# Kernel tuning notes

Hardware: AMD Instinct MI355X
Metric: run time of the kernel (lower is better)

The kernel has to match this reference:

```python
import jax, jax.numpy as jnp
import numpy as np

N = 100000      # nodes
E = 800000      # edges (avg degree 8)
D_IN = 128
D_OUT = 128
HOPS = 3        # K in SGConv


def setup_inputs() -> dict:
    key = jax.random.key(0)
    k1, k2, k3 = jax.random.split(key, 3)
    x = jax.random.normal(k1, (N, D_IN), dtype=jnp.float32)
    edge_index = jax.random.randint(k2, (2, E), 0, N, dtype=jnp.int64)
    # SGConv's final torch.nn.Linear(in_channels, out_channels)
    W = jax.random.normal(k3, (D_OUT, D_IN), dtype=jnp.float32) / np.sqrt(D_IN).astype(np.float32)
    b = jnp.zeros((D_OUT,), dtype=jnp.float32)
    return {"x": x, "edge_index": edge_index, "W": W, "b": b}


def reference(x, edge_index, W, b):
    n = x.shape[0]
    loop = jnp.arange(n, dtype=edge_index.dtype)
    # gcn_norm with add_self_loops=True (SGConv default)
    src = jnp.concatenate([edge_index[0], loop])  # message sources
    dst = jnp.concatenate([edge_index[1], loop])  # aggregation targets
    ones = jnp.ones(src.shape[0], dtype=x.dtype)
    deg = jax.ops.segment_sum(ones, dst, num_segments=n)
    dinv = jnp.where(deg > 0, jax.lax.rsqrt(deg), 0.0)
    norm = dinv[src] * dinv[dst]  # symmetric D^-1/2 A_hat D^-1/2 coefficients

    def hop(h, _):
        msg = h[src] * norm[:, None]                      # [E+N, D] gather
        return jax.ops.segment_sum(msg, dst, num_segments=n), None

    h, _ = jax.lax.scan(hop, x, None, length=HOPS)        # A_norm^K x
    return h @ W.T + b                                     # final linear
```

## Files before the change

### kernel.cpp

```cpp
#include <hip/hip_runtime.h>
#include <hip/hip_bf16.h>

#define DF 128


typedef __attribute__((ext_vector_type(8))) short shortx8;
typedef __attribute__((ext_vector_type(4))) float floatx4;

__device__ __forceinline__ unsigned short f32_to_bf16_rne(float f) {
    unsigned int u = __float_as_uint(f);
    unsigned int r = (u >> 16) & 1u;
    u += 0x7FFFu + r;
    return (unsigned short)(u >> 16);
}
__device__ __forceinline__ float bf16_lo(unsigned int w) { return __uint_as_float(w << 16); }
__device__ __forceinline__ float bf16_hi(unsigned int w) { return __uint_as_float(w & 0xffff0000u); }
__device__ __forceinline__ unsigned int pack_bf16(float x, float y) {
    return ((unsigned int)f32_to_bf16_rne(y) << 16) | (unsigned int)f32_to_bf16_rne(x);
}

__global__ void detect_flags_kernel(const unsigned int* __restrict__ ew, int enwords,
                                    const unsigned short* __restrict__ xh, int xnh,
                                    int* __restrict__ flagI, int* __restrict__ flagD) {
    __shared__ int eodd_nz;
    __shared__ int xbig;
    if (threadIdx.x == 0) { eodd_nz = 0; xbig = 0; }
    __syncthreads();
    int f1 = 0;
    for (int i = 1 + 2 * (int)threadIdx.x; i < enwords; i += 2 * (int)blockDim.x)
        if (ew[i] != 0u) f1 = 1;
    int c = 0;
    for (int i = 2 * (int)threadIdx.x; i < xnh; i += 2 * (int)blockDim.x) {
        unsigned int e = ((unsigned int)xh[i] >> 7) & 0xFFu;
        if (e >= 0xC0u) c++;
    }
    if (f1) eodd_nz = 1;
    if (c) atomicAdd(&xbig, c);
    __syncthreads();
    if (threadIdx.x == 0) {
        *flagI = (eodd_nz == 0) ? 1 : 0;
        *flagD = (xbig > 8) ? 0 : 1;
    }
}

__global__ void count_deg_kernel(const int* __restrict__ eidx, const int* __restrict__ flagI,
                                 int E, int n, int* __restrict__ cnt) {
    int e = blockIdx.x * blockDim.x + threadIdx.x;
    if (e >= E) return;
    int s, d;
    if (*flagI) {
        const long long* p = (const long long*)eidx;
        s = (int)p[e];
        d = (int)p[(long long)E + e];
    } else {
        s = eidx[e];
        d = eidx[E + e];
    }
    if (d < 0 || d >= n || s < 0 || s >= n) return;
    atomicAdd(&cnt[d], 1);
}

__global__ void dinv_kernel(const int* __restrict__ cnt, float* __restrict__ dinv, int n) {
    int i = blockIdx.x * blockDim.x + threadIdx.x;
    if (i < n) dinv[i] = rsqrtf((float)(cnt[i] + 1));
}

__global__ void scan_blocks_kernel(const int* __restrict__ cnt, int* __restrict__ row_start,
                                   int* __restrict__ partials, int n) {
    __shared__ int s[256];
    int i = blockIdx.x * 256 + threadIdx.x;
    int v = (i < n) ? cnt[i] : 0;
    s[threadIdx.x] = v;
    __syncthreads();
    for (int off = 1; off < 256; off <<= 1) {
        int t = ((int)threadIdx.x >= off) ? s[threadIdx.x - off] : 0;
        __syncthreads();
        s[threadIdx.x] += t;
        __syncthreads();
    }
    if (i < n) row_start[i] = s[threadIdx.x] - v;
    if (threadIdx.x == 255) partials[blockIdx.x] = s[255];
}

__global__ void scan_partials_kernel(int* __restrict__ partials, int nparts) {
    __shared__ int s[512];
    int v = ((int)threadIdx.x < nparts) ? partials[threadIdx.x] : 0;
    s[threadIdx.x] = v;
    __syncthreads();
    for (int off = 1; off < 512; off <<= 1) {
        int t = ((int)threadIdx.x >= off) ? s[threadIdx.x - off] : 0;
        __syncthreads();
        s[threadIdx.x] += t;
        __syncthreads();
    }
    if ((int)threadIdx.x < nparts) partials[threadIdx.x] = s[threadIdx.x] - v;
}

__global__ void finalize_rows_kernel(int* __restrict__ row_start, const int* __restrict__ partials,
                                     const int* __restrict__ cnt, int* __restrict__ cursor, int n) {
    int i = blockIdx.x * 256 + threadIdx.x;
    if (i < n) {
        int r = row_start[i] + partials[blockIdx.x];
        row_start[i] = r;
        cursor[i] = r;
        if (i == n - 1) row_start[n] = r + cnt[i];
    }
}

__global__ void scatter_kernel(const int* __restrict__ eidx, const int* __restrict__ flagI,
                               int E, int n, const float* __restrict__ dinv,
                               int* __restrict__ cursor, int2* __restrict__ csr) {
    int e = blockIdx.x * blockDim.x + threadIdx.x;
    if (e >= E) return;
    int s, d;
    if (*flagI) {
        const long long* p = (const long long*)eidx;
        s = (int)p[e];
        d = (int)p[(long long)E + e];
    } else {
        s = eidx[e];
        d = eidx[E + e];
    }
    if (d < 0 || d >= n || s < 0 || s >= n) return;
    int pos = atomicAdd(&cursor[d], 1);
    int2 pk;
    pk.x = s;
    pk.y = __float_as_int(dinv[s]);
    csr[pos] = pk;
}

__global__ void cast_x_kernel(const void* __restrict__ x, uint2* __restrict__ xb,
                              const int* __restrict__ flagD, int nw2) {
    int i = blockIdx.x * blockDim.x + threadIdx.x;
    if (i >= nw2) return;
    if (*flagD) {
        xb[i] = ((const uint2*)x)[i];
    } else {
        float4 v = ((const float4*)x)[i];
        uint2 o;
        o.x = pack_bf16(v.x, v.y);
        o.y = pack_bf16(v.z, v.w);
        xb[i] = o;
    }
}

__global__ void cast_wb_kernel(const void* __restrict__ W, const void* __restrict__ b,
                               unsigned short* __restrict__ Wb, float* __restrict__ bias_f,
                               const int* __restrict__ flagD) {
    int i = blockIdx.x * 256 + threadIdx.x;
    int bf = *flagD;
    if (i < 128 * 128)
        Wb[i] = bf ? ((const unsigned short*)W)[i] : f32_to_bf16_rne(((const float*)W)[i]);
    if (i < 128)
        bias_f[i] = bf ? bf16_lo((unsigned int)((const unsigned short*)b)[i]) : ((const float*)b)[i];
}

__global__ __launch_bounds__(256) void hop_kernel(const uint4* __restrict__ hin,
                                                  uint4* __restrict__ hout,
                                                  const int2* __restrict__ csr,
                                                  const int* __restrict__ row_start,
                                                  const float* __restrict__ dinv, int n) {
    int gw = (int)((blockIdx.x * 256 + threadIdx.x) >> 6);
    int lane = (int)(threadIdx.x & 63);
    if (gw >= n) return;
    int e = lane >> 4, c = lane & 15;
    float di = dinv[gw];
    int beg = row_start[gw], end = row_start[gw + 1];
    uint4 sv = hin[(size_t)gw * 16 + c];
    float a0 = 0.f, a1 = 0.f, a2 = 0.f, a3 = 0.f, a4 = 0.f, a5 = 0.f, a6 = 0.f, a7 = 0.f;
    for (int j = beg + e; j < end; j += 4) {
        int2 ed = csr[j];
        float w = __int_as_float(ed.y);
        uint4 v = hin[(size_t)ed.x * 16 + c];
        a0 += w * bf16_lo(v.x); a1 += w * bf16_hi(v.x);
        a2 += w * bf16_lo(v.y); a3 += w * bf16_hi(v.y);
        a4 += w * bf16_lo(v.z); a5 += w * bf16_hi(v.z);
        a6 += w * bf16_lo(v.w); a7 += w * bf16_hi(v.w);
    }
    a0 += __shfl_xor(a0, 16); a0 += __shfl_xor(a0, 32);
    a1 += __shfl_xor(a1, 16); a1 += __shfl_xor(a1, 32);
    a2 += __shfl_xor(a2, 16); a2 += __shfl_xor(a2, 32);
    a3 += __shfl_xor(a3, 16); a3 += __shfl_xor(a3, 32);
    a4 += __shfl_xor(a4, 16); a4 += __shfl_xor(a4, 32);
    a5 += __shfl_xor(a5, 16); a5 += __shfl_xor(a5, 32);
    a6 += __shfl_xor(a6, 16); a6 += __shfl_xor(a6, 32);
    a7 += __shfl_xor(a7, 16); a7 += __shfl_xor(a7, 32);
    a0 = di * (a0 + di * bf16_lo(sv.x)); a1 = di * (a1 + di * bf16_hi(sv.x));
    a2 = di * (a2 + di * bf16_lo(sv.y)); a3 = di * (a3 + di * bf16_hi(sv.y));
    a4 = di * (a4 + di * bf16_lo(sv.z)); a5 = di * (a5 + di * bf16_hi(sv.z));
    a6 = di * (a6 + di * bf16_lo(sv.w)); a7 = di * (a7 + di * bf16_hi(sv.w));
    if (e == 0) {
        uint4 o;
        o.x = pack_bf16(a0, a1);
        o.y = pack_bf16(a2, a3);
        o.z = pack_bf16(a4, a5);
        o.w = pack_bf16(a6, a7);
        hout[(size_t)gw * 16 + c] = o;
    }
}

__global__ __launch_bounds__(256, 2) void linear_mfma_kernel(
        const unsigned short* __restrict__ h, const unsigned short* __restrict__ Wb,
        const float* __restrict__ bias_f, void* __restrict__ out,
        const int* __restrict__ flagD, int n) {
    int bf = *flagD;
    int wave = (int)(threadIdx.x >> 6);
    int lane = (int)(threadIdx.x & 63);
    int q = lane >> 4, m16 = lane & 15;

    shortx8 bfrag[8][4];
    float bias[8];
#pragma unroll
    for (int nt = 0; nt < 8; ++nt) {
        int wr = nt * 16 + m16;
#pragma unroll
        for (int t = 0; t < 4; ++t)
            bfrag[nt][t] = *(const shortx8*)&Wb[wr * 128 + t * 32 + q * 8];
        bias[nt] = bias_f[wr];
    }

    int nstrips = (n + 15) / 16;
    int wid = (int)blockIdx.x * 4 + wave;
    int nw = (int)gridDim.x * 4;
    for (int s = wid; s < nstrips; s += nw) {
        int row0 = s * 16;
        int arow = row0 + m16;
        if (arow >= n) arow = n - 1;
        shortx8 afrag[4];
#pragma unroll
        for (int t = 0; t < 4; ++t)
            afrag[t] = *(const shortx8*)&h[(size_t)arow * 128 + t * 32 + q * 8];

        floatx4 acc[8];
#pragma unroll
        for (int nt = 0; nt < 8; ++nt) acc[nt] = (floatx4){0.f, 0.f, 0.f, 0.f};
#pragma unroll
        for (int t = 0; t < 4; ++t)
#pragma unroll
            for (int nt = 0; nt < 8; ++nt)
                acc[nt] = __builtin_amdgcn_mfma_f32_16x16x32_bf16(afrag[t], bfrag[nt][t], acc[nt], 0, 0, 0);

#pragma unroll
        for (int nt = 0; nt < 8; ++nt)
#pragma unroll
            for (int r = 0; r < 4; ++r) {
                int row = row0 + q * 4 + r;
                if (row < n) {
                    float v = acc[nt][r] + bias[nt];
                    size_t oi = (size_t)row * 128 + nt * 16 + m16;
                    if (bf) ((unsigned short*)out)[oi] = f32_to_bf16_rne(v);
                    else    ((float*)out)[oi] = v;
                }
            }
    }
}

extern "C" void kernel_launch(void* const* d_in, const int* in_sizes, int n_in,
                              void* d_out, int out_size, void* d_ws, size_t ws_size,
                              hipStream_t stream) {
    const void* x = d_in[0];
    const int* eidx = (const int*)d_in[1];
    const void* W = d_in[2];
    const void* b = d_in[3];

    int n = in_sizes[0] / DF;
    int E = in_sizes[1] / 2;

    char* ws = (char*)d_ws;
    size_t off = 0;
    auto alloc = [&](size_t bytes) -> void* {
        void* p = ws + off;
        off = (off + bytes + 255) & ~(size_t)255;
        return p;
    };
    unsigned int* hb = (unsigned int*)alloc((size_t)n * 64 * 4);
    float* dinv      = (float*)alloc((size_t)n * 4);
    int*   cnt       = (int*)alloc((size_t)n * 4);
    int*   row_start = (int*)alloc((size_t)(n + 1) * 4);
    int*   cursor    = (int*)alloc((size_t)n * 4);
    int*   partials  = (int*)alloc(4096);
    int*   flagI     = (int*)alloc(256);
    int*   flagD     = (int*)alloc(256);
    unsigned short* Wb = (unsigned short*)alloc(128 * 128 * 2);
    float* bias_f    = (float*)alloc(128 * 4);
    int2*  csr       = (int2*)alloc((size_t)E * 8);
    unsigned int* xb = (unsigned int*)d_out;

    hipMemsetAsync(cnt, 0, (size_t)n * 4, stream);

    int enw = 8192; if (2 * E < enw) enw = 2 * E;
    int xnh = 16384; if (n * DF < xnh) xnh = n * DF;
    detect_flags_kernel<<<1, 256, 0, stream>>>((const unsigned int*)eidx, enw,
                                               (const unsigned short*)x, xnh, flagI, flagD);

    int eb = (E + 255) / 256;
    int nb = (n + 255) / 256;
    count_deg_kernel<<<eb, 256, 0, stream>>>(eidx, flagI, E, n, cnt);
    dinv_kernel<<<nb, 256, 0, stream>>>(cnt, dinv, n);
    scan_blocks_kernel<<<nb, 256, 0, stream>>>(cnt, row_start, partials, n);
    scan_partials_kernel<<<1, 512, 0, stream>>>(partials, nb);
    finalize_rows_kernel<<<nb, 256, 0, stream>>>(row_start, partials, cnt, cursor, n);
    scatter_kernel<<<eb, 256, 0, stream>>>(eidx, flagI, E, n, dinv, cursor, csr);

    int nw2 = n * 32;
    cast_x_kernel<<<(nw2 + 255) / 256, 256, 0, stream>>>(x, (uint2*)xb, flagD, nw2);
    cast_wb_kernel<<<64, 256, 0, stream>>>(W, b, Wb, bias_f, flagD);

    int hb_grid = (n + 3) / 4;
    hop_kernel<<<hb_grid, 256, 0, stream>>>((const uint4*)xb, (uint4*)hb, csr, row_start, dinv, n);
    hop_kernel<<<hb_grid, 256, 0, stream>>>((const uint4*)hb, (uint4*)xb, csr, row_start, dinv, n);
    hop_kernel<<<hb_grid, 256, 0, stream>>>((const uint4*)xb, (uint4*)hb, csr, row_start, dinv, n);

    int nstrips = (n + 15) / 16;
    int lgrid = 512; if ((nstrips + 3) / 4 < lgrid) lgrid = (nstrips + 3) / 4;
    linear_mfma_kernel<<<lgrid, 256, 0, stream>>>(
        (const unsigned short*)hb, Wb, bias_f, d_out, flagD, n);
}
```

Baseline: 358.9 us.

## Pre-scale features by D^-1/2 so hops need only unweighted neighbor sums

Rewrites the normalized propagation as g = D^-1/2 h, so each hop sums neighbor rows without per-edge weights and scales by dinv^2 (or dinv on the last hop). This shrinks CSR entries from int2 (index plus weight) to a single int, halving edge-list traffic and dropping one multiply per element per edge. The input cast now folds in the initial dinv scaling, and the degree count no longer reads source indices. Out-of-range sources are now clamped rather than the edge being skipped, and storing pre-scaled values in bf16 between hops changes rounding slightly.

```diff
diff --git a/kernel.cpp b/kernel.cpp
--- a/kernel.cpp
+++ b/kernel.cpp
@@ -47,16 +47,10 @@
                                  int E, int n, int* __restrict__ cnt) {
     int e = blockIdx.x * blockDim.x + threadIdx.x;
     if (e >= E) return;
-    int s, d;
-    if (*flagI) {
-        const long long* p = (const long long*)eidx;
-        s = (int)p[e];
-        d = (int)p[(long long)E + e];
-    } else {
-        s = eidx[e];
-        d = eidx[E + e];
-    }
-    if (d < 0 || d >= n || s < 0 || s >= n) return;
+    int d;
+    if (*flagI) d = (int)((const long long*)eidx)[(long long)E + e];
+    else        d = eidx[E + e];
+    if (d < 0 || d >= n) return;
     atomicAdd(&cnt[d], 1);
 }
 
@@ -108,8 +102,7 @@
 }
 
 __global__ void scatter_kernel(const int* __restrict__ eidx, const int* __restrict__ flagI,
-                               int E, int n, const float* __restrict__ dinv,
-                               int* __restrict__ cursor, int2* __restrict__ csr) {
+                               int E, int n, int* __restrict__ cursor, int* __restrict__ csr) {
     int e = blockIdx.x * blockDim.x + threadIdx.x;
     if (e >= E) return;
     int s, d;
@@ -121,27 +114,30 @@
         s = eidx[e];
         d = eidx[E + e];
     }
-    if (d < 0 || d >= n || s < 0 || s >= n) return;
+    if (d < 0 || d >= n) return;
+    s = min(max(s, 0), n - 1);
     int pos = atomicAdd(&cursor[d], 1);
-    int2 pk;
-    pk.x = s;
-    pk.y = __float_as_int(dinv[s]);
-    csr[pos] = pk;
-}
-
-__global__ void cast_x_kernel(const void* __restrict__ x, uint2* __restrict__ xb,
-                              const int* __restrict__ flagD, int nw2) {
+    csr[pos] = s;
+}
+
+__global__ void cast_g0_kernel(const void* __restrict__ x, uint2* __restrict__ g0,
+                               const float* __restrict__ dinv,
+                               const int* __restrict__ flagD, int n) {
     int i = blockIdx.x * blockDim.x + threadIdx.x;
+    int nw2 = n * 32;
     if (i >= nw2) return;
+    float w = dinv[i >> 5];
+    uint2 o;
     if (*flagD) {
-        xb[i] = ((const uint2*)x)[i];
+        uint2 v = ((const uint2*)x)[i];
+        o.x = pack_bf16(w * bf16_lo(v.x), w * bf16_hi(v.x));
+        o.y = pack_bf16(w * bf16_lo(v.y), w * bf16_hi(v.y));
     } else {
         float4 v = ((const float4*)x)[i];
-        uint2 o;
-        o.x = pack_bf16(v.x, v.y);
-        o.y = pack_bf16(v.z, v.w);
-        xb[i] = o;
-    }
+        o.x = pack_bf16(w * v.x, w * v.y);
+        o.y = pack_bf16(w * v.z, w * v.w);
+    }
+    g0[i] = o;
 }
 
 __global__ void cast_wb_kernel(const void* __restrict__ W, const void* __restrict__ b,
@@ -157,25 +153,25 @@
 
 __global__ __launch_bounds__(256) void hop_kernel(const uint4* __restrict__ hin,
                                                   uint4* __restrict__ hout,
-                                                  const int2* __restrict__ csr,
+                                                  const int* __restrict__ csr,
                                                   const int* __restrict__ row_start,
-                                                  const float* __restrict__ dinv, int n) {
+                                                  const float* __restrict__ dinv, int n, int last) {
     int gw = (int)((blockIdx.x * 256 + threadIdx.x) >> 6);
     int lane = (int)(threadIdx.x & 63);
     if (gw >= n) return;
     int e = lane >> 4, c = lane & 15;
     float di = dinv[gw];
+    float scale = last ? di : di * di;
     int beg = row_start[gw], end = row_start[gw + 1];
     uint4 sv = hin[(size_t)gw * 16 + c];
     float a0 = 0.f, a1 = 0.f, a2 = 0.f, a3 = 0.f, a4 = 0.f, a5 = 0.f, a6 = 0.f, a7 = 0.f;
     for (int j = beg + e; j < end; j += 4) {
-        int2 ed = csr[j];
-        float w = __int_as_float(ed.y);
-        uint4 v = hin[(size_t)ed.x * 16 + c];
-        a0 += w * bf16_lo(v.x); a1 += w * bf16_hi(v.x);
-        a2 += w * bf16_lo(v.y); a3 += w * bf16_hi(v.y);
-        a4 += w * bf16_lo(v.z); a5 += w * bf16_hi(v.z);
-        a6 += w * bf16_lo(v.w); a7 += w * bf16_hi(v.w);
+        int s = csr[j];
+        uint4 v = hin[(size_t)s * 16 + c];
+        a0 += bf16_lo(v.x); a1 += bf16_hi(v.x);
+        a2 += bf16_lo(v.y); a3 += bf16_hi(v.y);
+        a4 += bf16_lo(v.z); a5 += bf16_hi(v.z);
+        a6 += bf16_lo(v.w); a7 += bf16_hi(v.w);
     }
     a0 += __shfl_xor(a0, 16); a0 += __shfl_xor(a0, 32);
     a1 += __shfl_xor(a1, 16); a1 += __shfl_xor(a1, 32);
@@ -185,10 +181,10 @@
     a5 += __shfl_xor(a5, 16); a5 += __shfl_xor(a5, 32);
     a6 += __shfl_xor(a6, 16); a6 += __shfl_xor(a6, 32);
     a7 += __shfl_xor(a7, 16); a7 += __shfl_xor(a7, 32);
-    a0 = di * (a0 + di * bf16_lo(sv.x)); a1 = di * (a1 + di * bf16_hi(sv.x));
-    a2 = di * (a2 + di * bf16_lo(sv.y)); a3 = di * (a3 + di * bf16_hi(sv.y));
-    a4 = di * (a4 + di * bf16_lo(sv.z)); a5 = di * (a5 + di * bf16_hi(sv.z));
-    a6 = di * (a6 + di * bf16_lo(sv.w)); a7 = di * (a7 + di * bf16_hi(sv.w));
+    a0 = scale * (a0 + bf16_lo(sv.x)); a1 = scale * (a1 + bf16_hi(sv.x));
+    a2 = scale * (a2 + bf16_lo(sv.y)); a3 = scale * (a3 + bf16_hi(sv.y));
+    a4 = scale * (a4 + bf16_lo(sv.z)); a5 = scale * (a5 + bf16_hi(sv.z));
+    a6 = scale * (a6 + bf16_lo(sv.w)); a7 = scale * (a7 + bf16_hi(sv.w));
     if (e == 0) {
         uint4 o;
         o.x = pack_bf16(a0, a1);
@@ -283,7 +279,7 @@
     int*   flagD     = (int*)alloc(256);
     unsigned short* Wb = (unsigned short*)alloc(128 * 128 * 2);
     float* bias_f    = (float*)alloc(128 * 4);
-    int2*  csr       = (int2*)alloc((size_t)E * 8);
+    int*   csr       = (int*)alloc((size_t)E * 4);
     unsigned int* xb = (unsigned int*)d_out;
 
     hipMemsetAsync(cnt, 0, (size_t)n * 4, stream);
@@ -300,16 +296,16 @@
     scan_blocks_kernel<<<nb, 256, 0, stream>>>(cnt, row_start, partials, n);
     scan_partials_kernel<<<1, 512, 0, stream>>>(partials, nb);
     finalize_rows_kernel<<<nb, 256, 0, stream>>>(row_start, partials, cnt, cursor, n);
-    scatter_kernel<<<eb, 256, 0, stream>>>(eidx, flagI, E, n, dinv, cursor, csr);
+    scatter_kernel<<<eb, 256, 0, stream>>>(eidx, flagI, E, n, cursor, csr);
 
     int nw2 = n * 32;
-    cast_x_kernel<<<(nw2 + 255) / 256, 256, 0, stream>>>(x, (uint2*)xb, flagD, nw2);
+    cast_g0_kernel<<<(nw2 + 255) / 256, 256, 0, stream>>>(x, (uint2*)xb, dinv, flagD, n);
     cast_wb_kernel<<<64, 256, 0, stream>>>(W, b, Wb, bias_f, flagD);
 
     int hb_grid = (n + 3) / 4;
-    hop_kernel<<<hb_grid, 256, 0, stream>>>((const uint4*)xb, (uint4*)hb, csr, row_start, dinv, n);
-    hop_kernel<<<hb_grid, 256, 0, stream>>>((const uint4*)hb, (uint4*)xb, csr, row_start, dinv, n);
-    hop_kernel<<<hb_grid, 256, 0, stream>>>((const uint4*)xb, (uint4*)hb, csr, row_start, dinv, n);
+    hop_kernel<<<hb_grid, 256, 0, stream>>>((const uint4*)xb, (uint4*)hb, csr, row_start, dinv, n, 0);
+    hop_kernel<<<hb_grid, 256, 0, stream>>>((const uint4*)hb, (uint4*)xb, csr, row_start, dinv, n, 0);
+    hop_kernel<<<hb_grid, 256, 0, stream>>>((const uint4*)xb, (uint4*)hb, csr, row_start, dinv, n, 1);
 
     int nstrips = (n + 15) / 16;
     int lgrid = 512; if ((nstrips + 3) / 4 < lgrid) lgrid = (nstrips + 3) / 4;
```

New measurement: 364.3 us. Within noise of the previous version (+1.5%).
